# Kernel tuning notes

Measured on AMD Instinct MI355X. Metric: run time of the kernel, lower is better.

The kernel has to match this reference:

```python
import jax, jax.numpy as jnp
import numpy as np
import math

B, N, IN_DIM, EMBED, HEADS = 1, 96, 128, 128, 4
HD = EMBED // HEADS  # head_dim = 32


def _layernorm(x, g, b, eps=1e-5):
    mu = jnp.mean(x, axis=-1, keepdims=True)
    var = jnp.var(x, axis=-1, keepdims=True)
    return (x - mu) * jax.lax.rsqrt(var + eps) * g + b


def setup_inputs() -> dict:
    key = jax.random.key(0)
    ks = jax.random.split(key, 3)
    x = jax.random.normal(ks[0], (B, N, N, IN_DIM), dtype=jnp.float32)
    W = jax.random.normal(ks[1], (IN_DIM, EMBED), dtype=jnp.float32) / math.sqrt(IN_DIM)
    b = jnp.zeros((EMBED,), jnp.float32)
    ln_g = jnp.ones((HD,), jnp.float32)
    ln_b = jnp.zeros((HD,), jnp.float32)
    Wf = jax.random.normal(ks[2], (IN_DIM + EMBED, EMBED), dtype=jnp.float32) / math.sqrt(IN_DIM + EMBED)
    bf = jnp.zeros((EMBED,), jnp.float32)
    ln2_g = jnp.ones((EMBED,), jnp.float32)
    ln2_b = jnp.zeros((EMBED,), jnp.float32)
    return {"x": x, "W": W, "b": b, "ln_g": ln_g, "ln_b": ln_b,
            "Wf": Wf, "bf": bf, "ln2_g": ln2_g, "ln2_b": ln2_b}


def reference(x, W, b, ln_g, ln_b, Wf, bf, ln2_g, ln2_b):
    # NOTE: original torch module shares ONE Linear across q/k/v1/v2 and ONE
    # LayerNorm across norms[0..2] (ModuleList([m]*k) aliases the module).
    Bq, Nq = x.shape[0], x.shape[1]
    p = (jnp.einsum('bxyi,ie->bxye', x, W) + b).reshape(Bq, Nq, Nq, HEADS, HD)
    pn = _layernorm(p, ln_g, ln_b)                         # q == k (shared params)
    scores = jnp.einsum('bxahd,bayhd->bxayh', pn, pn) / math.sqrt(HD)
    att = jax.nn.softmax(scores, axis=2)                   # softmax over a
    x_upd = jnp.einsum('bxahd,bayhd->bxayhd', p, p)        # v1 == v2 == p
    x_upd = _layernorm(x_upd, ln_g, ln_b)                  # shared norm params
    agg = jnp.einsum('bxayh,bxayhd->bxyhd', att, x_upd).reshape(Bq, Nq, Nq, EMBED)
    cat = jnp.concatenate([x, agg], axis=-1)
    out = jnp.einsum('bxyc,ce->bxye', cat, Wf) + bf
    return _layernorm(out, ln2_g, ln2_b)
```

## Files before the change

### kernel.cpp

```cpp
#include <hip/hip_runtime.h>
#include <math.h>

#define NTOK 96
#define EMBED 128
#define HEADS 4
#define HD 32
#define NROW (NTOK*NTOK)
#define YT 8
#define NYT (NTOK/YT)

__global__ __launch_bounds__(128) void k_proj(
    const float* __restrict__ x, const float* __restrict__ W,
    const float* __restrict__ b, const float* __restrict__ ln_g,
    const float* __restrict__ ln_b,
    float* __restrict__ pF, float4* __restrict__ murF) {
  const int r0 = blockIdx.x * 4;
  const int U  = r0 / NTOK;
  const int v0 = r0 % NTOK;
  const int e  = threadIdx.x;
  __shared__ float xt[EMBED][4];
  #pragma unroll
  for (int k = 0; k < 4; ++k)
    xt[e][k] = x[(size_t)(r0 + k) * EMBED + e];
  __syncthreads();

  const float bias = b[e];
  float a0 = bias, a1 = bias, a2 = bias, a3 = bias;
  #pragma unroll 8
  for (int i = 0; i < EMBED; ++i) {
    const float wv = W[(size_t)i * EMBED + e];
    const float4 c = *(const float4*)&xt[i][0];
    a0 = fmaf(wv, c.x, a0); a1 = fmaf(wv, c.y, a1);
    a2 = fmaf(wv, c.z, a2); a3 = fmaf(wv, c.w, a3);
  }

  const int h = e >> 5;
  const int d = e & 31;
  const float gl = ln_g[d];
  const float bl = ln_b[d];
  const float gl2 = gl * gl;
  const float gvb = gl * bl;
  float accs[4] = {a0, a1, a2, a3};
  #pragma unroll
  for (int k = 0; k < 4; ++k) {
    const float val = accs[k];
    const int v = v0 + k;
    pF[(((size_t)v * HEADS + h) * NTOK + U) * HD + d] = val;
    float s1 = val, s2 = val * val, s3 = gl2 * val, s4 = gvb * val;
    #pragma unroll
    for (int m_ = 1; m_ < 32; m_ <<= 1) {
      s1 += __shfl_xor(s1, m_, 64);
      s2 += __shfl_xor(s2, m_, 64);
      s3 += __shfl_xor(s3, m_, 64);
      s4 += __shfl_xor(s4, m_, 64);
    }
    if (d == 0) {
      const float mu = s1 * (1.f / HD);
      const float var = fmaxf(s2 * (1.f / HD) - mu * mu, 0.f);
      float4 o; o.x = mu; o.y = rsqrtf(var + 1e-5f); o.z = s3; o.w = s4;
      murF[((size_t)v * HEADS + h) * NTOK + U] = o;
    }
  }
}

#define PR_QUAD(E4, F4, G2, T4) \
  T4.x = E4.x * F4.x; sraw = fmaf(G2.x, T4.x, sraw); m += T4.x; q = fmaf(T4.x, T4.x, q); \
  T4.y = E4.y * F4.y; sraw = fmaf(G2.y, T4.y, sraw); m += T4.y; q = fmaf(T4.y, T4.y, q); \
  T4.z = E4.z * F4.z; sraw = fmaf(G2.z, T4.z, sraw); m += T4.z; q = fmaf(T4.z, T4.z, q); \
  T4.w = E4.w * F4.w; sraw = fmaf(G2.w, T4.w, sraw); m += T4.w; q = fmaf(T4.w, T4.w, q);

#define AGG_QUAD(A4, T4) \
  A4.x = fmaf(w, T4.x, A4.x); A4.y = fmaf(w, T4.y, A4.y); \
  A4.z = fmaf(w, T4.z, A4.z); A4.w = fmaf(w, T4.w, A4.w);

#define RED_QUAD(A4, MASK) \
  A4.x += __shfl_xor(A4.x, MASK, 64); A4.y += __shfl_xor(A4.y, MASK, 64); \
  A4.z += __shfl_xor(A4.z, MASK, 64); A4.w += __shfl_xor(A4.w, MASK, 64);

__global__ __launch_bounds__(256) void k_attn(
    const float* __restrict__ pF, const float4* __restrict__ murF,
    const float* __restrict__ ln_g, const float* __restrict__ ln_b,
    float* __restrict__ agg) {
  const int bid = blockIdx.x;
  const int X   = bid % NTOK;
  const int t2i = bid / NTOK;
  const int y0  = (t2i % NYT) * YT;
  const int H   = t2i / NYT;

  const int tid = threadIdx.x;
  const int y   = tid >> 5;
  const int ds  = (tid >> 4) & 1;
  const int da  = tid & 15;
  const int yy  = y0 + y;
  const int eoff = ds * 16;

  __shared__ float e_sm[NTOK][36];
  __shared__ float4 mur_sm[NTOK];

  #pragma unroll
  for (int i = 0; i < 3; ++i) {
    const int g = tid + i * 256;
    const int a = g >> 3, qq = g & 7;
    *(float4*)&e_sm[a][qq * 4] =
        *(const float4*)&pF[(((size_t)a * HEADS + H) * NTOK + X) * HD + qq * 4];
  }
  if (tid < NTOK)
    mur_sm[tid] = murF[((size_t)tid * HEADS + H) * NTOK + X];

  const float glx = ln_g[tid & 31];
  const float blx = ln_b[tid & 31];
  float T2c = glx * glx, Vbc = glx * blx, Wbc = blx * blx, Mg2 = glx * glx;
  #pragma unroll
  for (int m_ = 1; m_ < 32; m_ <<= 1) {
    T2c += __shfl_xor(T2c, m_, 64);
    Vbc += __shfl_xor(Vbc, m_, 64);
    Wbc += __shfl_xor(Wbc, m_, 64);
    Mg2 = fmaxf(Mg2, __shfl_xor(Mg2, m_, 64));
  }
  const float SB = (64.f * Mg2 + 2.f * Wbc) * 0.17677669529663687f;

  float4 g2q0, g2q1, g2q2, g2q3;
  {
    const float4 t0 = *(const float4*)&ln_g[eoff];
    const float4 t1 = *(const float4*)&ln_g[eoff + 4];
    const float4 t2 = *(const float4*)&ln_g[eoff + 8];
    const float4 t3 = *(const float4*)&ln_g[eoff + 12];
    g2q0.x = t0.x*t0.x; g2q0.y = t0.y*t0.y; g2q0.z = t0.z*t0.z; g2q0.w = t0.w*t0.w;
    g2q1.x = t1.x*t1.x; g2q1.y = t1.y*t1.y; g2q1.z = t1.z*t1.z; g2q1.w = t1.w*t1.w;
    g2q2.x = t2.x*t2.x; g2q2.y = t2.y*t2.y; g2q2.z = t2.z*t2.z; g2q2.w = t2.w*t2.w;
    g2q3.x = t3.x*t3.x; g2q3.y = t3.y*t3.y; g2q3.z = t3.z*t3.z; g2q3.w = t3.w*t3.w;
  }
  __syncthreads();

  const float* fbase = pF + (((size_t)yy * HEADS + H) * NTOK) * HD + eoff;
  const float4* mfb  = murF + ((size_t)yy * HEADS + H) * NTOK;

  float4 acc0 = {0,0,0,0}, acc1 = {0,0,0,0}, acc2 = {0,0,0,0}, acc3 = {0,0,0,0};
  float den = 0.f, cc = 0.f;

  #pragma unroll 2
  for (int ia = 0; ia < 6; ++ia) {
    const int a = ia * 16 + da;
    const float4* fp = (const float4*)(fbase + (size_t)a * HD);
    const float4 f0 = fp[0], f1 = fp[1], f2 = fp[2], f3 = fp[3];
    const float4 mrF = mfb[a];
    const float4 mrE = mur_sm[a];
    const float4 e0 = *(const float4*)&e_sm[a][eoff];
    const float4 e1 = *(const float4*)&e_sm[a][eoff + 4];
    const float4 e2 = *(const float4*)&e_sm[a][eoff + 8];
    const float4 e3 = *(const float4*)&e_sm[a][eoff + 12];

    float sraw = 0.f, m = 0.f, q = 0.f;
    float4 t0, t1, t2, t3;
    PR_QUAD(e0, f0, g2q0, t0);
    PR_QUAD(e1, f1, g2q1, t1);
    PR_QUAD(e2, f2, g2q2, t2);
    PR_QUAD(e3, f3, g2q3, t3);

    sraw += __shfl_xor(sraw, 16, 64);
    m    += __shfl_xor(m,    16, 64);
    q    += __shfl_xor(q,    16, 64);

    const float muE = mrE.x, rE = mrE.y, Sg2E = mrE.z, SgbE = mrE.w;
    const float muF = mrF.x, rF = mrF.y, Sg2F = mrF.z, SgbF = mrF.w;
    const float inner = sraw - muF * Sg2E - muE * Sg2F + muE * muF * T2c;
    const float sfull = rE * rF * inner
                      + rE * (SgbE - muE * Vbc)
                      + rF * (SgbF - muF * Vbc) + Wbc;
    const float sc = sfull * 0.17677669529663687f;

    const float mu = m * (1.f / HD);
    const float var = fmaxf(fmaf(-mu, mu, q * (1.f / HD)), 0.f);
    const float r = rsqrtf(var + 1e-5f);

    const float ex = __expf(sc - SB);
    const float w = ex * r;
    den += ex;
    cc  = fmaf(w, mu, cc);
    AGG_QUAD(acc0, t0);
    AGG_QUAD(acc1, t1);
    AGG_QUAD(acc2, t2);
    AGG_QUAD(acc3, t3);
  }

  #pragma unroll
  for (int mask = 1; mask <= 8; mask <<= 1) {
    den += __shfl_xor(den, mask, 64);
    cc  += __shfl_xor(cc,  mask, 64);
    RED_QUAD(acc0, mask);
    RED_QUAD(acc1, mask);
    RED_QUAD(acc2, mask);
    RED_QUAD(acc3, mask);
  }

  if (da == 0) {
    const float4 gq0 = *(const float4*)&ln_g[eoff];
    const float4 gq1 = *(const float4*)&ln_g[eoff + 4];
    const float4 gq2 = *(const float4*)&ln_g[eoff + 8];
    const float4 gq3 = *(const float4*)&ln_g[eoff + 12];
    const float4 bq0 = *(const float4*)&ln_b[eoff];
    const float4 bq1 = *(const float4*)&ln_b[eoff + 4];
    const float4 bq2 = *(const float4*)&ln_b[eoff + 8];
    const float4 bq3 = *(const float4*)&ln_b[eoff + 12];
    const float inv = 1.f / den;
    float4 o0, o1, o2, o3;
    o0.x = fmaf(gq0.x, (acc0.x - cc) * inv, bq0.x);
    o0.y = fmaf(gq0.y, (acc0.y - cc) * inv, bq0.y);
    o0.z = fmaf(gq0.z, (acc0.z - cc) * inv, bq0.z);
    o0.w = fmaf(gq0.w, (acc0.w - cc) * inv, bq0.w);
    o1.x = fmaf(gq1.x, (acc1.x - cc) * inv, bq1.x);
    o1.y = fmaf(gq1.y, (acc1.y - cc) * inv, bq1.y);
    o1.z = fmaf(gq1.z, (acc1.z - cc) * inv, bq1.z);
    o1.w = fmaf(gq1.w, (acc1.w - cc) * inv, bq1.w);
    o2.x = fmaf(gq2.x, (acc2.x - cc) * inv, bq2.x);
    o2.y = fmaf(gq2.y, (acc2.y - cc) * inv, bq2.y);
    o2.z = fmaf(gq2.z, (acc2.z - cc) * inv, bq2.z);
    o2.w = fmaf(gq2.w, (acc2.w - cc) * inv, bq2.w);
    o3.x = fmaf(gq3.x, (acc3.x - cc) * inv, bq3.x);
    o3.y = fmaf(gq3.y, (acc3.y - cc) * inv, bq3.y);
    o3.z = fmaf(gq3.z, (acc3.z - cc) * inv, bq3.z);
    o3.w = fmaf(gq3.w, (acc3.w - cc) * inv, bq3.w);
    float* op = agg + ((size_t)(X * NTOK + yy)) * EMBED + H * HD + eoff;
    *(float4*)&op[0]  = o0;
    *(float4*)&op[4]  = o1;
    *(float4*)&op[8]  = o2;
    *(float4*)&op[12] = o3;
  }
}

__global__ __launch_bounds__(256) void k_final(
    const float* __restrict__ x, const float* __restrict__ agg,
    const float* __restrict__ Wf, const float* __restrict__ bf,
    const float* __restrict__ g2, const float* __restrict__ b2,
    float* __restrict__ out) {
  const int r0 = blockIdx.x * 8;
  const int tid = threadIdx.x;
  const int e = tid & 127;
  const int rh = tid >> 7;
  __shared__ float ct[2 * EMBED][12];
  __shared__ float red_sm[4][4][2];

  #pragma unroll
  for (int i = 0; i < 8; ++i) {
    const int g = tid + i * 256;
    const int yl = g >> 8, col = g & 255;
    const size_t row = (size_t)(r0 + yl);
    const float v = (col < 128) ? x[row * EMBED + col]
                                : agg[row * EMBED + (col - 128)];
    ct[col][yl] = v;
  }
  __syncthreads();

  const float bias = bf[e];
  float acc4[4] = {bias, bias, bias, bias};
  #pragma unroll 8
  for (int i = 0; i < 2 * EMBED; ++i) {
    const float wv = Wf[(size_t)i * EMBED + e];
    const float4 c0 = *(const float4*)&ct[i][rh * 4];
    acc4[0] = fmaf(wv, c0.x, acc4[0]); acc4[1] = fmaf(wv, c0.y, acc4[1]);
    acc4[2] = fmaf(wv, c0.z, acc4[2]); acc4[3] = fmaf(wv, c0.w, acc4[3]);
  }

  const int wid = tid >> 6;
  #pragma unroll
  for (int k = 0; k < 4; ++k) {
    float s1 = acc4[k], s2 = acc4[k] * acc4[k];
    #pragma unroll
    for (int m_ = 1; m_ < 64; m_ <<= 1) {
      s1 += __shfl_xor(s1, m_, 64);
      s2 += __shfl_xor(s2, m_, 64);
    }
    if ((tid & 63) == 0) { red_sm[wid][k][0] = s1; red_sm[wid][k][1] = s2; }
  }
  __syncthreads();

  const float gg = g2[e], bb = b2[e];
  #pragma unroll
  for (int k = 0; k < 4; ++k) {
    const float S1 = red_sm[wid][k][0] + red_sm[wid ^ 1][k][0];
    const float S2 = red_sm[wid][k][1] + red_sm[wid ^ 1][k][1];
    const float mu = S1 * (1.f / EMBED);
    const float var = fmaxf(S2 * (1.f / EMBED) - mu * mu, 0.f);
    const float rstd = rsqrtf(var + 1e-5f);
    out[(size_t)(r0 + rh * 4 + k) * EMBED + e] = (acc4[k] - mu) * rstd * gg + bb;
  }
}

extern "C" void kernel_launch(void* const* d_in, const int* in_sizes, int n_in,
                              void* d_out, int out_size, void* d_ws, size_t ws_size,
                              hipStream_t stream) {
  const float* x    = (const float*)d_in[0];
  const float* W    = (const float*)d_in[1];
  const float* b    = (const float*)d_in[2];
  const float* ln_g = (const float*)d_in[3];
  const float* ln_b = (const float*)d_in[4];
  const float* Wf   = (const float*)d_in[5];
  const float* bf   = (const float*)d_in[6];
  const float* g2   = (const float*)d_in[7];
  const float* b2   = (const float*)d_in[8];
  float* out = (float*)d_out;

  float*  pF   = (float*)d_ws;
  float4* murF = (float4*)(pF + (size_t)NROW * EMBED);
  float*  agg  = (float*)(murF + (size_t)NROW * HEADS);

  k_proj<<<NROW / 4, 128, 0, stream>>>(x, W, b, ln_g, ln_b, pF, murF);
  k_attn<<<NTOK * NYT * HEADS, 256, 0, stream>>>(pF, murF, ln_g, ln_b, agg);
  k_final<<<NROW / 8, 256, 0, stream>>>(x, agg, Wf, bf, g2, b2, out);
}
```

Before: 111.0 us.

## Double attention y-tile to 16 and read per-X LN stats from transposed buffer

The attention kernel now handles 16 y values per block with 512 threads instead of 8 with 256. This halves the number of blocks and reuses each shared e_sm tile across more outputs. The projection kernel also writes a second, transposed copy of the LayerNorm statistics (murE), so the attention kernel reads them coalesced from global memory instead of staging them in shared memory. The cost is an extra scattered global write in the projection kernel, more workspace, and fewer but larger blocks, which may lower occupancy.

Measured after the change: 112.5 us. Within noise of the previous version (+1.4%).

```diff
diff --git a/kernel.cpp b/kernel.cpp
--- a/kernel.cpp
+++ b/kernel.cpp
@@ -6,14 +6,15 @@
 #define HEADS 4
 #define HD 32
 #define NROW (NTOK*NTOK)
-#define YT 8
+#define YT 16
 #define NYT (NTOK/YT)
 
 __global__ __launch_bounds__(128) void k_proj(
     const float* __restrict__ x, const float* __restrict__ W,
     const float* __restrict__ b, const float* __restrict__ ln_g,
     const float* __restrict__ ln_b,
-    float* __restrict__ pF, float4* __restrict__ murF) {
+    float* __restrict__ pF, float4* __restrict__ murF,
+    float4* __restrict__ murE) {
   const int r0 = blockIdx.x * 4;
   const int U  = r0 / NTOK;
   const int v0 = r0 % NTOK;
@@ -59,6 +60,7 @@
       const float var = fmaxf(s2 * (1.f / HD) - mu * mu, 0.f);
       float4 o; o.x = mu; o.y = rsqrtf(var + 1e-5f); o.z = s3; o.w = s4;
       murF[((size_t)v * HEADS + h) * NTOK + U] = o;
+      murE[((size_t)U * HEADS + h) * NTOK + v] = o;
     }
   }
 }
@@ -77,8 +79,9 @@
   A4.x += __shfl_xor(A4.x, MASK, 64); A4.y += __shfl_xor(A4.y, MASK, 64); \
   A4.z += __shfl_xor(A4.z, MASK, 64); A4.w += __shfl_xor(A4.w, MASK, 64);
 
-__global__ __launch_bounds__(256) void k_attn(
+__global__ __launch_bounds__(512) void k_attn(
     const float* __restrict__ pF, const float4* __restrict__ murF,
+    const float4* __restrict__ murE,
     const float* __restrict__ ln_g, const float* __restrict__ ln_b,
     float* __restrict__ agg) {
   const int bid = blockIdx.x;
@@ -95,17 +98,19 @@
   const int eoff = ds * 16;
 
   __shared__ float e_sm[NTOK][36];
-  __shared__ float4 mur_sm[NTOK];
-
-  #pragma unroll
-  for (int i = 0; i < 3; ++i) {
-    const int g = tid + i * 256;
-    const int a = g >> 3, qq = g & 7;
+
+  {
+    const int g0 = tid;
+    const int a = g0 >> 3, qq = g0 & 7;
     *(float4*)&e_sm[a][qq * 4] =
         *(const float4*)&pF[(((size_t)a * HEADS + H) * NTOK + X) * HD + qq * 4];
   }
-  if (tid < NTOK)
-    mur_sm[tid] = murF[((size_t)tid * HEADS + H) * NTOK + X];
+  if (tid < 256) {
+    const int g1 = tid + 512;
+    const int a = g1 >> 3, qq = g1 & 7;
+    *(float4*)&e_sm[a][qq * 4] =
+        *(const float4*)&pF[(((size_t)a * HEADS + H) * NTOK + X) * HD + qq * 4];
+  }
 
   const float glx = ln_g[tid & 31];
   const float blx = ln_b[tid & 31];
@@ -132,8 +137,9 @@
   }
   __syncthreads();
 
-  const float* fbase = pF + (((size_t)yy * HEADS + H) * NTOK) * HD + eoff;
-  const float4* mfb  = murF + ((size_t)yy * HEADS + H) * NTOK;
+  const float* fbase  = pF + (((size_t)yy * HEADS + H) * NTOK) * HD + eoff;
+  const float4* mfb   = murF + ((size_t)yy * HEADS + H) * NTOK;
+  const float4* meb   = murE + ((size_t)X * HEADS + H) * NTOK;
 
   float4 acc0 = {0,0,0,0}, acc1 = {0,0,0,0}, acc2 = {0,0,0,0}, acc3 = {0,0,0,0};
   float den = 0.f, cc = 0.f;
@@ -144,7 +150,7 @@
     const float4* fp = (const float4*)(fbase + (size_t)a * HD);
     const float4 f0 = fp[0], f1 = fp[1], f2 = fp[2], f3 = fp[3];
     const float4 mrF = mfb[a];
-    const float4 mrE = mur_sm[a];
+    const float4 mrE = meb[a];
     const float4 e0 = *(const float4*)&e_sm[a][eoff];
     const float4 e1 = *(const float4*)&e_sm[a][eoff + 4];
     const float4 e2 = *(const float4*)&e_sm[a][eoff + 8];
@@ -302,9 +308,10 @@
 
   float*  pF   = (float*)d_ws;
   float4* murF = (float4*)(pF + (size_t)NROW * EMBED);
-  float*  agg  = (float*)(murF + (size_t)NROW * HEADS);
-
-  k_proj<<<NROW / 4, 128, 0, stream>>>(x, W, b, ln_g, ln_b, pF, murF);
-  k_attn<<<NTOK * NYT * HEADS, 256, 0, stream>>>(pF, murF, ln_g, ln_b, agg);
+  float4* murE = murF + (size_t)NROW * HEADS;
+  float*  agg  = (float*)(murE + (size_t)NROW * HEADS);
+
+  k_proj<<<NROW / 4, 128, 0, stream>>>(x, W, b, ln_g, ln_b, pF, murF, murE);
+  k_attn<<<NTOK * NYT * HEADS, 512, 0, stream>>>(pF, murF, murE, ln_g, ln_b, agg);
   k_final<<<NROW / 8, 256, 0, stream>>>(x, agg, Wf, bf, g2, b2, out);
 }
```

## Give each attn lane a full head-dim row and precompute transposed LN stats

Applied to the files above, without the earlier changes.

The attention kernel now maps each of the 32 lanes per y to a distinct 'a' index covering all 32 head dims, rather than splitting head dim across lane pairs. This removes the per-iteration cross-lane shuffle for scores and stats, but doubles accumulator registers and widens the final reduction to five steps. The projection kernel also writes a second, transposed copy of the per-row LN statistics, so the attention kernel reads them contiguously from global memory instead of staging them in shared memory. The cost is higher register pressure, which may reduce occupancy, plus extra global writes in the projection kernel.

Result: no change. 111.8 us (+0.8%).

```diff
diff --git a/kernel.cpp b/kernel.cpp
--- a/kernel.cpp
+++ b/kernel.cpp
@@ -13,7 +13,8 @@
     const float* __restrict__ x, const float* __restrict__ W,
     const float* __restrict__ b, const float* __restrict__ ln_g,
     const float* __restrict__ ln_b,
-    float* __restrict__ pF, float4* __restrict__ murF) {
+    float* __restrict__ pF, float4* __restrict__ murF,
+    float4* __restrict__ murE) {
   const int r0 = blockIdx.x * 4;
   const int U  = r0 / NTOK;
   const int v0 = r0 % NTOK;
@@ -59,26 +60,14 @@
       const float var = fmaxf(s2 * (1.f / HD) - mu * mu, 0.f);
       float4 o; o.x = mu; o.y = rsqrtf(var + 1e-5f); o.z = s3; o.w = s4;
       murF[((size_t)v * HEADS + h) * NTOK + U] = o;
-    }
-  }
-}
-
-#define PR_QUAD(E4, F4, G2, T4) \
-  T4.x = E4.x * F4.x; sraw = fmaf(G2.x, T4.x, sraw); m += T4.x; q = fmaf(T4.x, T4.x, q); \
-  T4.y = E4.y * F4.y; sraw = fmaf(G2.y, T4.y, sraw); m += T4.y; q = fmaf(T4.y, T4.y, q); \
-  T4.z = E4.z * F4.z; sraw = fmaf(G2.z, T4.z, sraw); m += T4.z; q = fmaf(T4.z, T4.z, q); \
-  T4.w = E4.w * F4.w; sraw = fmaf(G2.w, T4.w, sraw); m += T4.w; q = fmaf(T4.w, T4.w, q);
-
-#define AGG_QUAD(A4, T4) \
-  A4.x = fmaf(w, T4.x, A4.x); A4.y = fmaf(w, T4.y, A4.y); \
-  A4.z = fmaf(w, T4.z, A4.z); A4.w = fmaf(w, T4.w, A4.w);
-
-#define RED_QUAD(A4, MASK) \
-  A4.x += __shfl_xor(A4.x, MASK, 64); A4.y += __shfl_xor(A4.y, MASK, 64); \
-  A4.z += __shfl_xor(A4.z, MASK, 64); A4.w += __shfl_xor(A4.w, MASK, 64);
+      murE[((size_t)U * HEADS + h) * NTOK + v] = o;
+    }
+  }
+}
 
 __global__ __launch_bounds__(256) void k_attn(
     const float* __restrict__ pF, const float4* __restrict__ murF,
+    const float4* __restrict__ murE,
     const float* __restrict__ ln_g, const float* __restrict__ ln_b,
     float* __restrict__ agg) {
   const int bid = blockIdx.x;
@@ -89,13 +78,10 @@
 
   const int tid = threadIdx.x;
   const int y   = tid >> 5;
-  const int ds  = (tid >> 4) & 1;
-  const int da  = tid & 15;
+  const int da  = tid & 31;
   const int yy  = y0 + y;
-  const int eoff = ds * 16;
 
   __shared__ float e_sm[NTOK][36];
-  __shared__ float4 mur_sm[NTOK];
 
   #pragma unroll
   for (int i = 0; i < 3; ++i) {
@@ -104,8 +90,6 @@
     *(float4*)&e_sm[a][qq * 4] =
         *(const float4*)&pF[(((size_t)a * HEADS + H) * NTOK + X) * HD + qq * 4];
   }
-  if (tid < NTOK)
-    mur_sm[tid] = murF[((size_t)tid * HEADS + H) * NTOK + X];
 
   const float glx = ln_g[tid & 31];
   const float blx = ln_b[tid & 31];
@@ -119,47 +103,50 @@
   }
   const float SB = (64.f * Mg2 + 2.f * Wbc) * 0.17677669529663687f;
 
-  float4 g2q0, g2q1, g2q2, g2q3;
-  {
-    const float4 t0 = *(const float4*)&ln_g[eoff];
-    const float4 t1 = *(const float4*)&ln_g[eoff + 4];
-    const float4 t2 = *(const float4*)&ln_g[eoff + 8];
-    const float4 t3 = *(const float4*)&ln_g[eoff + 12];
-    g2q0.x = t0.x*t0.x; g2q0.y = t0.y*t0.y; g2q0.z = t0.z*t0.z; g2q0.w = t0.w*t0.w;
-    g2q1.x = t1.x*t1.x; g2q1.y = t1.y*t1.y; g2q1.z = t1.z*t1.z; g2q1.w = t1.w*t1.w;
-    g2q2.x = t2.x*t2.x; g2q2.y = t2.y*t2.y; g2q2.z = t2.z*t2.z; g2q2.w = t2.w*t2.w;
-    g2q3.x = t3.x*t3.x; g2q3.y = t3.y*t3.y; g2q3.z = t3.z*t3.z; g2q3.w = t3.w*t3.w;
-  }
-  __syncthreads();
-
-  const float* fbase = pF + (((size_t)yy * HEADS + H) * NTOK) * HD + eoff;
+  float g2c[32];
+  #pragma unroll
+  for (int d = 0; d < 32; ++d) { const float g = ln_g[d]; g2c[d] = g * g; }
+  __syncthreads();
+
+  const float* fbase = pF + (((size_t)yy * HEADS + H) * NTOK) * HD;
   const float4* mfb  = murF + ((size_t)yy * HEADS + H) * NTOK;
-
-  float4 acc0 = {0,0,0,0}, acc1 = {0,0,0,0}, acc2 = {0,0,0,0}, acc3 = {0,0,0,0};
+  const float4* meb  = murE + ((size_t)X * HEADS + H) * NTOK;
+
+  float4 acc[8];
+  #pragma unroll
+  for (int k = 0; k < 8; ++k) acc[k] = make_float4(0.f, 0.f, 0.f, 0.f);
   float den = 0.f, cc = 0.f;
 
-  #pragma unroll 2
-  for (int ia = 0; ia < 6; ++ia) {
-    const int a = ia * 16 + da;
+  #pragma unroll
+  for (int ia = 0; ia < 3; ++ia) {
+    const int a = ia * 32 + da;
     const float4* fp = (const float4*)(fbase + (size_t)a * HD);
-    const float4 f0 = fp[0], f1 = fp[1], f2 = fp[2], f3 = fp[3];
+    float4 f[8], e[8], t[8];
+    #pragma unroll
+    for (int k = 0; k < 8; ++k) f[k] = fp[k];
     const float4 mrF = mfb[a];
-    const float4 mrE = mur_sm[a];
-    const float4 e0 = *(const float4*)&e_sm[a][eoff];
-    const float4 e1 = *(const float4*)&e_sm[a][eoff + 4];
-    const float4 e2 = *(const float4*)&e_sm[a][eoff + 8];
-    const float4 e3 = *(const float4*)&e_sm[a][eoff + 12];
-
-    float sraw = 0.f, m = 0.f, q = 0.f;
-    float4 t0, t1, t2, t3;
-    PR_QUAD(e0, f0, g2q0, t0);
-    PR_QUAD(e1, f1, g2q1, t1);
-    PR_QUAD(e2, f2, g2q2, t2);
-    PR_QUAD(e3, f3, g2q3, t3);
-
-    sraw += __shfl_xor(sraw, 16, 64);
-    m    += __shfl_xor(m,    16, 64);
-    q    += __shfl_xor(q,    16, 64);
+    const float4 mrE = meb[a];
+    #pragma unroll
+    for (int k = 0; k < 8; ++k) e[k] = *(const float4*)&e_sm[a][k * 4];
+
+    float s0 = 0.f, s1 = 0.f, m0 = 0.f, m1 = 0.f, q0 = 0.f, q1 = 0.f;
+    #pragma unroll
+    for (int k = 0; k < 4; ++k) {
+      t[k].x = e[k].x * f[k].x; s0 = fmaf(g2c[k*4+0], t[k].x, s0); m0 += t[k].x; q0 = fmaf(t[k].x, t[k].x, q0);
+      t[k].y = e[k].y * f[k].y; s0 = fmaf(g2c[k*4+1], t[k].y, s0); m0 += t[k].y; q0 = fmaf(t[k].y, t[k].y, q0);
+      t[k].z = e[k].z * f[k].z; s0 = fmaf(g2c[k*4+2], t[k].z, s0); m0 += t[k].z; q0 = fmaf(t[k].z, t[k].z, q0);
+      t[k].w = e[k].w * f[k].w; s0 = fmaf(g2c[k*4+3], t[k].w, s0); m0 += t[k].w; q0 = fmaf(t[k].w, t[k].w, q0);
+    }
+    #pragma unroll
+    for (int k = 4; k < 8; ++k) {
+      t[k].x = e[k].x * f[k].x; s1 = fmaf(g2c[k*4+0], t[k].x, s1); m1 += t[k].x; q1 = fmaf(t[k].x, t[k].x, q1);
+      t[k].y = e[k].y * f[k].y; s1 = fmaf(g2c[k*4+1], t[k].y, s1); m1 += t[k].y; q1 = fmaf(t[k].y, t[k].y, q1);
+      t[k].z = e[k].z * f[k].z; s1 = fmaf(g2c[k*4+2], t[k].z, s1); m1 += t[k].z; q1 = fmaf(t[k].z, t[k].z, q1);
+      t[k].w = e[k].w * f[k].w; s1 = fmaf(g2c[k*4+3], t[k].w, s1); m1 += t[k].w; q1 = fmaf(t[k].w, t[k].w, q1);
+    }
+    const float sraw = s0 + s1;
+    const float msum = m0 + m1;
+    const float qsum = q0 + q1;
 
     const float muE = mrE.x, rE = mrE.y, Sg2E = mrE.z, SgbE = mrE.w;
     const float muF = mrF.x, rF = mrF.y, Sg2F = mrF.z, SgbF = mrF.w;
@@ -169,62 +156,50 @@
                       + rF * (SgbF - muF * Vbc) + Wbc;
     const float sc = sfull * 0.17677669529663687f;
 
-    const float mu = m * (1.f / HD);
-    const float var = fmaxf(fmaf(-mu, mu, q * (1.f / HD)), 0.f);
+    const float mu = msum * (1.f / HD);
+    const float var = fmaxf(fmaf(-mu, mu, qsum * (1.f / HD)), 0.f);
     const float r = rsqrtf(var + 1e-5f);
 
     const float ex = __expf(sc - SB);
     const float w = ex * r;
     den += ex;
     cc  = fmaf(w, mu, cc);
-    AGG_QUAD(acc0, t0);
-    AGG_QUAD(acc1, t1);
-    AGG_QUAD(acc2, t2);
-    AGG_QUAD(acc3, t3);
-  }
-
-  #pragma unroll
-  for (int mask = 1; mask <= 8; mask <<= 1) {
+    #pragma unroll
+    for (int k = 0; k < 8; ++k) {
+      acc[k].x = fmaf(w, t[k].x, acc[k].x);
+      acc[k].y = fmaf(w, t[k].y, acc[k].y);
+      acc[k].z = fmaf(w, t[k].z, acc[k].z);
+      acc[k].w = fmaf(w, t[k].w, acc[k].w);
+    }
+  }
+
+  #pragma unroll
+  for (int mask = 1; mask <= 16; mask <<= 1) {
     den += __shfl_xor(den, mask, 64);
     cc  += __shfl_xor(cc,  mask, 64);
-    RED_QUAD(acc0, mask);
-    RED_QUAD(acc1, mask);
-    RED_QUAD(acc2, mask);
-    RED_QUAD(acc3, mask);
+    #pragma unroll
+    for (int k = 0; k < 8; ++k) {
+      acc[k].x += __shfl_xor(acc[k].x, mask, 64);
+      acc[k].y += __shfl_xor(acc[k].y, mask, 64);
+      acc[k].z += __shfl_xor(acc[k].z, mask, 64);
+      acc[k].w += __shfl_xor(acc[k].w, mask, 64);
+    }
   }
 
   if (da == 0) {
-    const float4 gq0 = *(const float4*)&ln_g[eoff];
-    const float4 gq1 = *(const float4*)&ln_g[eoff + 4];
-    const float4 gq2 = *(const float4*)&ln_g[eoff + 8];
-    const float4 gq3 = *(const float4*)&ln_g[eoff + 12];
-    const float4 bq0 = *(const float4*)&ln_b[eoff];
-    const float4 bq1 = *(const float4*)&ln_b[eoff + 4];
-    const float4 bq2 = *(const float4*)&ln_b[eoff + 8];
-    const float4 bq3 = *(const float4*)&ln_b[eoff + 12];
     const float inv = 1.f / den;
-    float4 o0, o1, o2, o3;
-    o0.x = fmaf(gq0.x, (acc0.x - cc) * inv, bq0.x);
-    o0.y = fmaf(gq0.y, (acc0.y - cc) * inv, bq0.y);
-    o0.z = fmaf(gq0.z, (acc0.z - cc) * inv, bq0.z);
-    o0.w = fmaf(gq0.w, (acc0.w - cc) * inv, bq0.w);
-    o1.x = fmaf(gq1.x, (acc1.x - cc) * inv, bq1.x);
-    o1.y = fmaf(gq1.y, (acc1.y - cc) * inv, bq1.y);
-    o1.z = fmaf(gq1.z, (acc1.z - cc) * inv, bq1.z);
-    o1.w = fmaf(gq1.w, (acc1.w - cc) * inv, bq1.w);
-    o2.x = fmaf(gq2.x, (acc2.x - cc) * inv, bq2.x);
-    o2.y = fmaf(gq2.y, (acc2.y - cc) * inv, bq2.y);
-    o2.z = fmaf(gq2.z, (acc2.z - cc) * inv, bq2.z);
-    o2.w = fmaf(gq2.w, (acc2.w - cc) * inv, bq2.w);
-    o3.x = fmaf(gq3.x, (acc3.x - cc) * inv, bq3.x);
-    o3.y = fmaf(gq3.y, (acc3.y - cc) * inv, bq3.y);
-    o3.z = fmaf(gq3.z, (acc3.z - cc) * inv, bq3.z);
-    o3.w = fmaf(gq3.w, (acc3.w - cc) * inv, bq3.w);
-    float* op = agg + ((size_t)(X * NTOK + yy)) * EMBED + H * HD + eoff;
-    *(float4*)&op[0]  = o0;
-    *(float4*)&op[4]  = o1;
-    *(float4*)&op[8]  = o2;
-    *(float4*)&op[12] = o3;
+    float* op = agg + ((size_t)(X * NTOK + yy)) * EMBED + H * HD;
+    #pragma unroll
+    for (int k = 0; k < 8; ++k) {
+      const float4 gq = *(const float4*)&ln_g[k * 4];
+      const float4 bq = *(const float4*)&ln_b[k * 4];
+      float4 o;
+      o.x = fmaf(gq.x, (acc[k].x - cc) * inv, bq.x);
+      o.y = fmaf(gq.y, (acc[k].y - cc) * inv, bq.y);
+      o.z = fmaf(gq.z, (acc[k].z - cc) * inv, bq.z);
+      o.w = fmaf(gq.w, (acc[k].w - cc) * inv, bq.w);
+      *(float4*)&op[k * 4] = o;
+    }
   }
 }
 
@@ -302,9 +277,10 @@
 
   float*  pF   = (float*)d_ws;
   float4* murF = (float4*)(pF + (size_t)NROW * EMBED);
-  float*  agg  = (float*)(murF + (size_t)NROW * HEADS);
-
-  k_proj<<<NROW / 4, 128, 0, stream>>>(x, W, b, ln_g, ln_b, pF, murF);
-  k_attn<<<NTOK * NYT * HEADS, 256, 0, stream>>>(pF, murF, ln_g, ln_b, agg);
+  float4* murE = murF + (size_t)NROW * HEADS;
+  float*  agg  = (float*)(murE + (size_t)NROW * HEADS);
+
+  k_proj<<<NROW / 4, 128, 0, stream>>>(x, W, b, ln_g, ln_b, pF, murF, murE);
+  k_attn<<<NTOK * NYT * HEADS, 256, 0, stream>>>(pF, murF, murE, ln_g, ln_b, agg);
   k_final<<<NROW / 8, 256, 0, stream>>>(x, agg, Wf, bf, g2, b2, out);
 }
```
